# Kernel optimization log

Measured on AMD Instinct MI355X. Metric: run time of the kernel, lower is better.

## Reference

```python
import jax, jax.numpy as jnp
import numpy as np

ALPHA = 0.3
D_K = 64


def setup_inputs() -> dict:
    key = jax.random.key(0)
    kq, kk, kv = jax.random.split(key, 3)
    B, H, S, D = 4, 16, 2048, 64
    Q = jax.random.normal(kq, (B, H, S, D), dtype=jnp.float32)
    K = jax.random.normal(kk, (B, H, S, D), dtype=jnp.float32)
    V = jax.random.normal(kv, (B, H, S, D), dtype=jnp.float32)
    attn_mask = jnp.zeros((B, H, S, S), dtype=bool)
    return {"Q": Q, "K": K, "V": V, "attn_mask": attn_mask}


def reference(Q, K, V, attn_mask):
    # scores: [B,H,S,S] = QK^T / sqrt(d_k)
    scores = jnp.einsum("bhqd,bhkd->bhqk", Q, K) / np.sqrt(D_K).astype(np.float32)
    # adj_tanh(x, a) = (e^{ax}-e^{-ax})/(e^{ax}+e^{-ax}) == tanh(a*x)
    attn = jnp.tanh(ALPHA * scores)
    # NOTE: original torch code calls attn.masked_fill(...) (non in-place) and
    # discards the result, so the mask has NO effect on the output. Replicated
    # faithfully: attn_mask is accepted but unused.
    context = jnp.einsum("bhqk,bhkd->bhqd", attn, V)
    return context
```

## Files before the change

kernel.cpp:

```cpp
#include <hip/hip_runtime.h>


constexpr int S_LEN = 2048;
constexpr int DIM   = 64;
constexpr int QT    = 256;
constexpr int KT    = 64;
constexpr int NKT   = S_LEN / KT;

constexpr float C_EXP2 = 0.10820212528f;

typedef __bf16 bf16_t;
typedef bf16_t bf16x4 __attribute__((ext_vector_type(4)));
typedef bf16_t bf16x8 __attribute__((ext_vector_type(8)));
typedef float  f32x4  __attribute__((ext_vector_type(4)));

__device__ inline bf16x8 to_bf8(float4 a, float4 b) {
    bf16x8 v;
    v[0] = (bf16_t)a.x; v[1] = (bf16_t)a.y; v[2] = (bf16_t)a.z; v[3] = (bf16_t)a.w;
    v[4] = (bf16_t)b.x; v[5] = (bf16_t)b.y; v[6] = (bf16_t)b.z; v[7] = (bf16_t)b.w;
    return v;
}

__global__ __launch_bounds__(512, 4) void tanh_attn_kernel(
    const float* __restrict__ Q, const float* __restrict__ K,
    const float* __restrict__ V, float* __restrict__ O)
{
    const int tid  = threadIdx.x;
    const int lane = tid & 63;
    const int wv   = tid >> 6;
    const int lr   = lane & 15;
    const int lg   = lane >> 4;

    const int nwg = gridDim.x;
    const int bid = (blockIdx.x & 7) * (nwg >> 3) + (blockIdx.x >> 3);
    const int qtile = bid & 7;
    const int bh    = bid >> 3;
    const int base  = bh * (S_LEN * DIM);
    const int q0    = qtile * QT;

    __shared__ bf16_t Ql[QT * DIM];
    __shared__ bf16_t Kl[2][KT * DIM];
    __shared__ bf16_t Vt[2][DIM * KT];

    const float* Kb = K + base;
    const float* Vb = V + base;

    const int sr  = tid >> 3;
    const int sc8 = (tid & 7) * 8;
    const int sd  = tid & 63;
    const int skv = (tid >> 6) * 8;

    float4 ka, kb2;
    float  vv[8];
    {
        const float* src = Kb + sr * DIM + sc8;
        ka  = *(const float4*)src;
        kb2 = *(const float4*)(src + 4);
        const float* vsrc = Vb + skv * DIM + sd;
        #pragma unroll
        for (int j = 0; j < 8; ++j) vv[j] = vsrc[j * DIM];
    }

    #pragma unroll
    for (int it = 0; it < 4; ++it) {
        int cid = tid + it * 512;
        int r   = cid >> 3;
        int c8  = (cid & 7) * 8;
        const float* src = Q + base + (q0 + r) * DIM + c8;
        float4 a = *(const float4*)src;
        float4 b = *(const float4*)(src + 4);
        *(bf16x8*)&Ql[r * DIM + (c8 ^ ((r & 7) << 3))] = to_bf8(a, b);
    }
    __syncthreads();

    bf16x8 qa[2][2];
    #pragma unroll
    for (int rt = 0; rt < 2; ++rt)
        #pragma unroll
        for (int ks = 0; ks < 2; ++ks) {
            int r = wv * 32 + rt * 16 + lr;
            int c = ks * 32 + lg * 8;
            qa[rt][ks] = *(const bf16x8*)&Ql[r * DIM + (c ^ ((r & 7) << 3))];
        }

    {
        *(bf16x8*)&Kl[0][sr * DIM + (sc8 ^ ((sr & 7) << 3))] = to_bf8(ka, kb2);
        bf16x8 v;
        #pragma unroll
        for (int j = 0; j < 8; ++j) v[j] = (bf16_t)vv[j];
        *(bf16x8*)&Vt[0][sd * KT + (skv ^ ((sd & 7) << 3))] = v;
    }

    f32x4 oacc[2][4] = {};
    bf16_t* Pl = Ql + wv * (32 * KT);

    #pragma unroll 2
    for (int kt = 0; kt < NKT; ++kt) {
        const int cur = kt & 1;

        __syncthreads();

        if (kt + 1 < NKT) {
            const int k0n = (kt + 1) * KT;
            const float* src = Kb + (k0n + sr) * DIM + sc8;
            ka  = *(const float4*)src;
            kb2 = *(const float4*)(src + 4);
            const float* vsrc = Vb + (k0n + skv) * DIM + sd;
            #pragma unroll
            for (int j = 0; j < 8; ++j) vv[j] = vsrc[j * DIM];
        }

        const bf16_t* Kc = Kl[cur];
        const bf16_t* Vc = Vt[cur];

        f32x4 sacc[2][4] = {};
        __builtin_amdgcn_s_setprio(1);
        #pragma unroll
        for (int ct = 0; ct < 4; ++ct) {
            int r = ct * 16 + lr;
            bf16x8 kf0 = *(const bf16x8*)&Kc[r * DIM + ((lg * 8)      ^ ((r & 7) << 3))];
            bf16x8 kf1 = *(const bf16x8*)&Kc[r * DIM + ((32 + lg * 8) ^ ((r & 7) << 3))];
            #pragma unroll
            for (int rt = 0; rt < 2; ++rt) {
                sacc[rt][ct] = __builtin_amdgcn_mfma_f32_16x16x32_bf16(kf0, qa[rt][0], sacc[rt][ct], 0, 0, 0);
                sacc[rt][ct] = __builtin_amdgcn_mfma_f32_16x16x32_bf16(kf1, qa[rt][1], sacc[rt][ct], 0, 0, 0);
            }
        }
        __builtin_amdgcn_s_setprio(0);

        #pragma unroll
        for (int rt = 0; rt < 2; ++rt)
            #pragma unroll
            for (int ct = 0; ct < 4; ++ct) {
                bf16x4 p4;
                #pragma unroll
                for (int j = 0; j < 4; ++j) {
                    float t = __builtin_amdgcn_exp2f(sacc[rt][ct][j] * C_EXP2);
                    p4[j] = (bf16_t)(1.0f - 2.0f * __builtin_amdgcn_rcpf(t + 1.0f));
                }
                int q  = rt * 16 + lr;
                int c0 = ct * 16 + lg * 4;
                *(bf16x4*)&Pl[q * KT + (c0 ^ ((q & 7) << 3))] = p4;
            }

        bf16x8 pa[2][2];
        #pragma unroll
        for (int rt = 0; rt < 2; ++rt)
            #pragma unroll
            for (int ks = 0; ks < 2; ++ks) {
                int r = rt * 16 + lr;
                pa[rt][ks] = *(const bf16x8*)&Pl[r * KT + ((ks * 32 + lg * 8) ^ ((r & 7) << 3))];
            }

        __builtin_amdgcn_s_setprio(1);
        #pragma unroll
        for (int dt = 0; dt < 4; ++dt) {
            int d = dt * 16 + lr;
            bf16x8 vf0 = *(const bf16x8*)&Vc[d * KT + ((lg * 8)      ^ ((d & 7) << 3))];
            bf16x8 vf1 = *(const bf16x8*)&Vc[d * KT + ((32 + lg * 8) ^ ((d & 7) << 3))];
            #pragma unroll
            for (int rt = 0; rt < 2; ++rt) {
                oacc[rt][dt] = __builtin_amdgcn_mfma_f32_16x16x32_bf16(pa[rt][0], vf0, oacc[rt][dt], 0, 0, 0);
                oacc[rt][dt] = __builtin_amdgcn_mfma_f32_16x16x32_bf16(pa[rt][1], vf1, oacc[rt][dt], 0, 0, 0);
            }
        }
        __builtin_amdgcn_s_setprio(0);

        if (kt + 1 < NKT) {
            const int nxt = cur ^ 1;
            *(bf16x8*)&Kl[nxt][sr * DIM + (sc8 ^ ((sr & 7) << 3))] = to_bf8(ka, kb2);
            bf16x8 v;
            #pragma unroll
            for (int j = 0; j < 8; ++j) v[j] = (bf16_t)vv[j];
            *(bf16x8*)&Vt[nxt][sd * KT + (skv ^ ((sd & 7) << 3))] = v;
        }
    }

    #pragma unroll
    for (int rt = 0; rt < 2; ++rt)
        #pragma unroll
        for (int dt = 0; dt < 4; ++dt)
            #pragma unroll
            for (int j = 0; j < 4; ++j) {
                int q = q0 + wv * 32 + rt * 16 + lg * 4 + j;
                int d = dt * 16 + lr;
                O[base + q * DIM + d] = oacc[rt][dt][j];
            }
}

extern "C" void kernel_launch(void* const* d_in, const int* in_sizes, int n_in,
                              void* d_out, int out_size, void* d_ws, size_t ws_size,
                              hipStream_t stream) {
    const float* Q = (const float*)d_in[0];
    const float* K = (const float*)d_in[1];
    const float* V = (const float*)d_in[2];
    float* O = (float*)d_out;
    dim3 grid(64 * (S_LEN / QT));
    dim3 block(512);
    hipLaunchKernelGGL(tanh_attn_kernel, grid, block, 0, stream, Q, K, V, O);
}
```

Measured before the change: 104.8 us.

## Keep P in registers via permlane swaps and use Pade tanh approximation

Drops the LDS round trip that reshaped the tanh-activated scores into the A-operand layout for the PV MFMA. The layout change is now done in registers with v_permlane32_swap/v_permlane16_swap, and the float-to-bf16 packing uses v_cvt_pk_bf16_f32. The exp2+rcp tanh is replaced by a clamped rational Pade approximation with the alpha/sqrt(dk) scale folded into its coefficients. This cuts LDS traffic and per-element transcendental ops, but relies on the cross-lane permute matching the MFMA layout and on the approximation staying accurate enough.

```diff
diff --git a/kernel.cpp b/kernel.cpp
--- a/kernel.cpp
+++ b/kernel.cpp
@@ -7,10 +7,7 @@
 constexpr int KT    = 64;
 constexpr int NKT   = S_LEN / KT;
 
-constexpr float C_EXP2 = 0.10820212528f;
-
 typedef __bf16 bf16_t;
-typedef bf16_t bf16x4 __attribute__((ext_vector_type(4)));
 typedef bf16_t bf16x8 __attribute__((ext_vector_type(8)));
 typedef float  f32x4  __attribute__((ext_vector_type(4)));
 
@@ -19,6 +16,26 @@
     v[0] = (bf16_t)a.x; v[1] = (bf16_t)a.y; v[2] = (bf16_t)a.z; v[3] = (bf16_t)a.w;
     v[4] = (bf16_t)b.x; v[5] = (bf16_t)b.y; v[6] = (bf16_t)b.z; v[7] = (bf16_t)b.w;
     return v;
+}
+
+__device__ inline float tanh_pade(float s) {
+    const float c1 = 7.41577148437e-08f;
+    const float c2 = 5.53710937500e-03f;
+    const float c3 = 35.4375f;
+    const float c4 = 2.96630859375e-05f;
+    const float c5 = 0.590625f;
+    float u = s * s;
+    float n = __builtin_fmaf(u, __builtin_fmaf(u, c1, c2), c3);
+    float d = __builtin_fmaf(u, __builtin_fmaf(u, c4, c5), 945.0f);
+    float r = (s * n) * __builtin_amdgcn_rcpf(d);
+    return fminf(1.0f, fmaxf(-1.0f, r));
+}
+
+__device__ inline void permlane32_swap(unsigned &a, unsigned &b) {
+    asm("v_permlane32_swap_b32 %0, %1" : "+v"(a), "+v"(b));
+}
+__device__ inline void permlane16_swap(unsigned &a, unsigned &b) {
+    asm("v_permlane16_swap_b32 %0, %1" : "+v"(a), "+v"(b));
 }
 
 __global__ __launch_bounds__(512, 4) void tanh_attn_kernel(
@@ -92,7 +109,6 @@
     }
 
     f32x4 oacc[2][4] = {};
-    bf16_t* Pl = Ql + wv * (32 * KT);
 
     #pragma unroll 2
     for (int kt = 0; kt < NKT; ++kt) {
@@ -128,29 +144,34 @@
         }
         __builtin_amdgcn_s_setprio(0);
 
-        #pragma unroll
-        for (int rt = 0; rt < 2; ++rt)
+        bf16x8 pa[2][2];
+        #pragma unroll
+        for (int rt = 0; rt < 2; ++rt) {
+            unsigned dm[4][2];
             #pragma unroll
             for (int ct = 0; ct < 4; ++ct) {
-                bf16x4 p4;
+                float p0 = tanh_pade(sacc[rt][ct][0]);
+                float p1 = tanh_pade(sacc[rt][ct][1]);
+                float p2 = tanh_pade(sacc[rt][ct][2]);
+                float p3 = tanh_pade(sacc[rt][ct][3]);
+                asm("v_cvt_pk_bf16_f32 %0, %1, %2" : "=v"(dm[ct][0]) : "v"(p0), "v"(p1));
+                asm("v_cvt_pk_bf16_f32 %0, %1, %2" : "=v"(dm[ct][1]) : "v"(p2), "v"(p3));
+            }
+            #pragma unroll
+            for (int ks = 0; ks < 2; ++ks) {
+                union { unsigned u[4]; bf16x8 v; } pw;
                 #pragma unroll
-                for (int j = 0; j < 4; ++j) {
-                    float t = __builtin_amdgcn_exp2f(sacc[rt][ct][j] * C_EXP2);
-                    p4[j] = (bf16_t)(1.0f - 2.0f * __builtin_amdgcn_rcpf(t + 1.0f));
+                for (int jj = 0; jj < 2; ++jj) {
+                    unsigned A = dm[2 * ks][jj];
+                    unsigned B = dm[2 * ks + 1][jj];
+                    permlane32_swap(A, B);
+                    permlane16_swap(A, B);
+                    pw.u[jj]     = A;
+                    pw.u[2 + jj] = B;
                 }
-                int q  = rt * 16 + lr;
-                int c0 = ct * 16 + lg * 4;
-                *(bf16x4*)&Pl[q * KT + (c0 ^ ((q & 7) << 3))] = p4;
-            }
-
-        bf16x8 pa[2][2];
-        #pragma unroll
-        for (int rt = 0; rt < 2; ++rt)
-            #pragma unroll
-            for (int ks = 0; ks < 2; ++ks) {
-                int r = rt * 16 + lr;
-                pa[rt][ks] = *(const bf16x8*)&Pl[r * KT + ((ks * 32 + lg * 8) ^ ((r & 7) << 3))];
-            }
+                pa[rt][ks] = pw.v;
+            }
+        }
 
         __builtin_amdgcn_s_setprio(1);
         #pragma unroll
```

After: 124.9 us. +19.2%, slower.

## Process two K/V tiles per barrier with quad-buffered LDS, load Q directly

Applied to the files above, without the earlier changes.

Switches from double to quad buffering of K/V tiles in shared memory so that each barrier covers two key tiles, halving the number of __syncthreads calls. Q fragments are now loaded straight from global memory into registers, which removes the Q staging buffer and the initial barrier. The per-wave P scratch is shrunk to 16 rows and reused across row tiles. LDS use changes from about 48KB to about 80KB, which may limit occupancy, and the register pressure pattern shifts.

```diff
diff --git a/kernel.cpp b/kernel.cpp
--- a/kernel.cpp
+++ b/kernel.cpp
@@ -6,6 +6,7 @@
 constexpr int QT    = 256;
 constexpr int KT    = 64;
 constexpr int NKT   = S_LEN / KT;
+constexpr int NW    = NKT / 2;
 
 constexpr float C_EXP2 = 0.10820212528f;
 
@@ -19,6 +20,11 @@
     v[0] = (bf16_t)a.x; v[1] = (bf16_t)a.y; v[2] = (bf16_t)a.z; v[3] = (bf16_t)a.w;
     v[4] = (bf16_t)b.x; v[5] = (bf16_t)b.y; v[6] = (bf16_t)b.z; v[7] = (bf16_t)b.w;
     return v;
+}
+
+__device__ inline float tanh_fast(float s) {
+    float t = __builtin_amdgcn_exp2f(s * C_EXP2);
+    return 1.0f - 2.0f * __builtin_amdgcn_rcpf(t + 1.0f);
 }
 
 __global__ __launch_bounds__(512, 4) void tanh_attn_kernel(
@@ -38,9 +44,9 @@
     const int base  = bh * (S_LEN * DIM);
     const int q0    = qtile * QT;
 
-    __shared__ bf16_t Ql[QT * DIM];
-    __shared__ bf16_t Kl[2][KT * DIM];
-    __shared__ bf16_t Vt[2][DIM * KT];
+    __shared__ bf16_t Kl[4][KT * DIM];
+    __shared__ bf16_t Vt[4][DIM * KT];
+    __shared__ bf16_t Pl[8][16 * KT];
 
     const float* Kb = K + base;
     const float* Vb = V + base;
@@ -52,6 +58,7 @@
 
     float4 ka, kb2;
     float  vv[8];
+
     {
         const float* src = Kb + sr * DIM + sc8;
         ka  = *(const float4*)src;
@@ -61,26 +68,16 @@
         for (int j = 0; j < 8; ++j) vv[j] = vsrc[j * DIM];
     }
 
-    #pragma unroll
-    for (int it = 0; it < 4; ++it) {
-        int cid = tid + it * 512;
-        int r   = cid >> 3;
-        int c8  = (cid & 7) * 8;
-        const float* src = Q + base + (q0 + r) * DIM + c8;
-        float4 a = *(const float4*)src;
-        float4 b = *(const float4*)(src + 4);
-        *(bf16x8*)&Ql[r * DIM + (c8 ^ ((r & 7) << 3))] = to_bf8(a, b);
-    }
-    __syncthreads();
-
     bf16x8 qa[2][2];
     #pragma unroll
     for (int rt = 0; rt < 2; ++rt)
         #pragma unroll
         for (int ks = 0; ks < 2; ++ks) {
-            int r = wv * 32 + rt * 16 + lr;
-            int c = ks * 32 + lg * 8;
-            qa[rt][ks] = *(const bf16x8*)&Ql[r * DIM + (c ^ ((r & 7) << 3))];
+            const float* src = Q + base + (q0 + wv * 32 + rt * 16 + lr) * DIM
+                               + ks * 32 + lg * 8;
+            float4 a = *(const float4*)src;
+            float4 b = *(const float4*)(src + 4);
+            qa[rt][ks] = to_bf8(a, b);
         }
 
     {
@@ -90,29 +87,25 @@
         for (int j = 0; j < 8; ++j) v[j] = (bf16_t)vv[j];
         *(bf16x8*)&Vt[0][sd * KT + (skv ^ ((sd & 7) << 3))] = v;
     }
+    {
+        const float* src = Kb + (KT + sr) * DIM + sc8;
+        ka  = *(const float4*)src;
+        kb2 = *(const float4*)(src + 4);
+        const float* vsrc = Vb + (KT + skv) * DIM + sd;
+        #pragma unroll
+        for (int j = 0; j < 8; ++j) vv[j] = vsrc[j * DIM];
+        *(bf16x8*)&Kl[1][sr * DIM + (sc8 ^ ((sr & 7) << 3))] = to_bf8(ka, kb2);
+        bf16x8 v;
+        #pragma unroll
+        for (int j = 0; j < 8; ++j) v[j] = (bf16_t)vv[j];
+        *(bf16x8*)&Vt[1][sd * KT + (skv ^ ((sd & 7) << 3))] = v;
+    }
 
     f32x4 oacc[2][4] = {};
-    bf16_t* Pl = Ql + wv * (32 * KT);
-
-    #pragma unroll 2
-    for (int kt = 0; kt < NKT; ++kt) {
-        const int cur = kt & 1;
-
-        __syncthreads();
-
-        if (kt + 1 < NKT) {
-            const int k0n = (kt + 1) * KT;
-            const float* src = Kb + (k0n + sr) * DIM + sc8;
-            ka  = *(const float4*)src;
-            kb2 = *(const float4*)(src + 4);
-            const float* vsrc = Vb + (k0n + skv) * DIM + sd;
-            #pragma unroll
-            for (int j = 0; j < 8; ++j) vv[j] = vsrc[j * DIM];
-        }
-
-        const bf16_t* Kc = Kl[cur];
-        const bf16_t* Vc = Vt[cur];
-
+    bf16_t* Pw = &Pl[wv][0];
+
+    auto compute = [&](const bf16_t* __restrict__ Kc,
+                       const bf16_t* __restrict__ Vc) {
         f32x4 sacc[2][4] = {};
         __builtin_amdgcn_s_setprio(1);
         #pragma unroll
@@ -128,29 +121,22 @@
         }
         __builtin_amdgcn_s_setprio(0);
 
-        #pragma unroll
-        for (int rt = 0; rt < 2; ++rt)
+        bf16x8 pa[2][2];
+        #pragma unroll
+        for (int rt = 0; rt < 2; ++rt) {
             #pragma unroll
             for (int ct = 0; ct < 4; ++ct) {
                 bf16x4 p4;
                 #pragma unroll
-                for (int j = 0; j < 4; ++j) {
-                    float t = __builtin_amdgcn_exp2f(sacc[rt][ct][j] * C_EXP2);
-                    p4[j] = (bf16_t)(1.0f - 2.0f * __builtin_amdgcn_rcpf(t + 1.0f));
-                }
-                int q  = rt * 16 + lr;
+                for (int j = 0; j < 4; ++j)
+                    p4[j] = (bf16_t)tanh_fast(sacc[rt][ct][j]);
                 int c0 = ct * 16 + lg * 4;
-                *(bf16x4*)&Pl[q * KT + (c0 ^ ((q & 7) << 3))] = p4;
-            }
-
-        bf16x8 pa[2][2];
-        #pragma unroll
-        for (int rt = 0; rt < 2; ++rt)
-            #pragma unroll
-            for (int ks = 0; ks < 2; ++ks) {
-                int r = rt * 16 + lr;
-                pa[rt][ks] = *(const bf16x8*)&Pl[r * KT + ((ks * 32 + lg * 8) ^ ((r & 7) << 3))];
-            }
+                *(bf16x4*)&Pw[lr * KT + (c0 ^ ((lr & 7) << 3))] = p4;
+            }
+            #pragma unroll
+            for (int ks = 0; ks < 2; ++ks)
+                pa[rt][ks] = *(const bf16x8*)&Pw[lr * KT + ((ks * 32 + lg * 8) ^ ((lr & 7) << 3))];
+        }
 
         __builtin_amdgcn_s_setprio(1);
         #pragma unroll
@@ -165,14 +151,50 @@
             }
         }
         __builtin_amdgcn_s_setprio(0);
-
-        if (kt + 1 < NKT) {
-            const int nxt = cur ^ 1;
-            *(bf16x8*)&Kl[nxt][sr * DIM + (sc8 ^ ((sr & 7) << 3))] = to_bf8(ka, kb2);
+    };
+
+    for (int w = 0; w < NW; ++w) {
+        const int p  = (w & 1) * 2;
+        const int np = p ^ 2;
+        const int t2 = 2 * w + 2, t3 = 2 * w + 3;
+
+        __syncthreads();
+
+        if (t2 < NKT) {
+            const float* src = Kb + (t2 * KT + sr) * DIM + sc8;
+            ka  = *(const float4*)src;
+            kb2 = *(const float4*)(src + 4);
+            const float* vsrc = Vb + (t2 * KT + skv) * DIM + sd;
+            #pragma unroll
+            for (int j = 0; j < 8; ++j) vv[j] = vsrc[j * DIM];
+        }
+
+        compute(Kl[p], Vt[p]);
+
+        if (t2 < NKT) {
+            *(bf16x8*)&Kl[np][sr * DIM + (sc8 ^ ((sr & 7) << 3))] = to_bf8(ka, kb2);
             bf16x8 v;
             #pragma unroll
             for (int j = 0; j < 8; ++j) v[j] = (bf16_t)vv[j];
-            *(bf16x8*)&Vt[nxt][sd * KT + (skv ^ ((sd & 7) << 3))] = v;
+            *(bf16x8*)&Vt[np][sd * KT + (skv ^ ((sd & 7) << 3))] = v;
+        }
+        if (t3 < NKT) {
+            const float* src = Kb + (t3 * KT + sr) * DIM + sc8;
+            ka  = *(const float4*)src;
+            kb2 = *(const float4*)(src + 4);
+            const float* vsrc = Vb + (t3 * KT + skv) * DIM + sd;
+            #pragma unroll
+            for (int j = 0; j < 8; ++j) vv[j] = vsrc[j * DIM];
+        }
+
+        compute(Kl[p + 1], Vt[p + 1]);
+
+        if (t3 < NKT) {
+            *(bf16x8*)&Kl[np + 1][sr * DIM + (sc8 ^ ((sr & 7) << 3))] = to_bf8(ka, kb2);
+            bf16x8 v;
+            #pragma unroll
+            for (int j = 0; j < 8; ++j) v[j] = (bf16_t)vv[j];
+            *(bf16x8*)&Vt[np + 1][sd * KT + (skv ^ ((sd & 7) << 3))] = v;
         }
     }
 
```

Result: slower. 108.7 us (+3.7%).
